# Performance work log

Measured on AMD Instinct MI355X. Metric: run time of the kernel, lower is better.

The kernel has to match this reference:

```python
import jax, jax.numpy as jnp
import numpy as np

EPS = 1e-15


def _trace(t):
    return jnp.einsum('bii->b', t)


def _ortho_loss(ss, k):
    n = jnp.linalg.norm(ss, axis=(-1, -2), keepdims=True)
    diff = ss / n - jnp.eye(k, dtype=ss.dtype) / np.float32(np.sqrt(k))
    return jnp.mean(jnp.linalg.norm(diff, axis=(-1, -2)))


def _mincut_terms(s, adj):
    out_adj = jnp.einsum('bnk,bnm,bml->bkl', s, adj, s)
    d_flat = adj.sum(-1)  # degrees [B,N]
    num = _trace(out_adj)
    den = _trace(jnp.einsum('bnk,bn,bnl->bkl', s, d_flat, s)) + EPS
    return out_adj, num, den, d_flat


def dense_mincut_rewiring(x, adj, s, mask):
    k = s.shape[-1]  # 2
    m = mask[..., None].astype(x.dtype)
    s = jax.nn.softmax(s, axis=-1) * m
    _, num, den, _ = _mincut_terms(s, adj)
    mincut_loss = -jnp.mean(num / den)
    ortho_loss = _ortho_loss(jnp.einsum('bnk,bnl->bkl', s, s), k)
    # laplacian derivative of spectral gap wrt A_uv: (f_u - f_v)^2, f = soft bipartition
    f = s[..., 0]
    dlam = (f[:, :, None] - f[:, None, :]) ** 2
    return adj * (1.0 - dlam), mincut_loss, ortho_loss


def dense_CT_rewiring(x, adj, s, mask):
    k = s.shape[-1]
    m = mask[..., None].astype(x.dtype)
    s = jax.nn.softmax(s, axis=-1) * m
    d_flat = adj.sum(-1)
    sds = _trace(jnp.einsum('bnk,bn,bnl->bkl', s, d_flat, s))
    sas = _trace(jnp.einsum('bnk,bnm,bml->bkl', s, adj, s))
    den = _trace(jnp.einsum('bnk,bnl->bkl', s, s)) + EPS
    ct_loss = jnp.mean((sds - sas) / den)  # tr(Z^T L Z) / tr(Z^T Z)
    ortho_loss = _ortho_loss(jnp.einsum('bnk,bnl->bkl', s, s), k)
    # pairwise CT distances ||z_u - z_v|| / vol(G), sparsified by A
    sq = (s * s).sum(-1)
    d2 = sq[:, :, None] + sq[:, None, :] - 2.0 * jnp.einsum('bnk,bmk->bnm', s, s)
    ct_dist = jnp.sqrt(jnp.maximum(d2, 0.0) + 1e-12)
    vol = d_flat.sum(-1)
    new_adj = (ct_dist / (vol[:, None, None] + EPS)) * adj
    return new_adj, ct_loss, ortho_loss


def dense_mincut_pool(x, adj, s, mask):
    k = s.shape[-1]
    m = mask[..., None].astype(x.dtype)
    s = jax.nn.softmax(s, axis=-1) * m
    x = x * m
    out = jnp.einsum('bnk,bnf->bkf', s, x)
    out_adj, num, den, _ = _mincut_terms(s, adj)
    mincut_loss = -jnp.mean(num / den)
    ortho_loss = _ortho_loss(jnp.einsum('bnk,bnl->bkl', s, s), k)
    out_adj = out_adj * (1.0 - jnp.eye(k, dtype=adj.dtype))  # zero diagonal
    d = jnp.sqrt(out_adj.sum(-1)) + EPS  # [B,k]
    out_adj = out_adj / d[:, None, :] / d[:, :, None]
    return out, out_adj, mincut_loss, ortho_loss


def _dgc(x, adj, w_rel, b_rel, w_root):
    # DenseGraphConv(aggr='add'): lin_rel(A @ x) + lin_root(x)
    return jnp.matmul(adj, x) @ w_rel + b_rel + x @ w_root


def setup_inputs() -> dict:
    B, N, IN, H, KC, OUT, KMC = 16, 1024, 128, 32, 32, 10, 16
    keys = iter(jax.random.split(jax.random.key(0), 48))

    def lin(fin, fout):
        lim = float(1.0 / np.sqrt(fin))
        return (jax.random.uniform(next(keys), (fin, fout), jnp.float32, -lim, lim),
                jax.random.uniform(next(keys), (fout,), jnp.float32, -lim, lim))

    x = jax.random.normal(next(keys), (B, N, IN), jnp.float32)
    u = jax.random.uniform(next(keys), (B, N, N), jnp.float32)
    a = (u < 0.0156).astype(jnp.float32)  # avg degree ~16
    adj = jnp.maximum(a, jnp.swapaxes(a, 1, 2)) * (1.0 - jnp.eye(N, dtype=jnp.float32))
    mask = jnp.ones((B, N), dtype=bool)
    W1, b1 = lin(IN, H)
    Wrw, brw = lin(H, 2)
    Wg_rel, bg = lin(H, H); Wg_root, _ = lin(H, H)
    Wmcg, bmcg = lin(H, KMC)
    W2g_rel, b2g = lin(H, H); W2g_root, _ = lin(H, H)
    Wct, bct = lin(H, KC)
    Wc_rel, bc = lin(H, H); Wc_root, _ = lin(H, H)
    Wmcc, bmcc = lin(H, KMC)
    Wcat, bcat = lin(2 * H, H)
    W2, b2 = lin(H, H)
    W3, b3 = lin(H, OUT)
    return dict(x=x, adj=adj, mask=mask, W1=W1, b1=b1, Wrw=Wrw, brw=brw,
                Wg_rel=Wg_rel, bg=bg, Wg_root=Wg_root, Wmcg=Wmcg, bmcg=bmcg,
                W2g_rel=W2g_rel, b2g=b2g, W2g_root=W2g_root, Wct=Wct, bct=bct,
                Wc_rel=Wc_rel, bc=bc, Wc_root=Wc_root, Wmcc=Wmcc, bmcc=bmcc,
                Wcat=Wcat, bcat=bcat, W2=W2, b2=b2, W3=W3, b3=b3)


def reference(x, adj, mask, W1, b1, Wrw, brw, Wg_rel, bg, Wg_root, Wmcg, bmcg,
              W2g_rel, b2g, W2g_root, Wct, bct, Wc_rel, bc, Wc_root, Wmcc, bmcc,
              Wcat, bcat, W2, b2, W3, b3):
    x = x @ W1 + b1
    # GAP branch
    adj_gap, mc_rw, ol_rw = dense_mincut_rewiring(x, adj, x @ Wrw + brw, mask)
    x_gap = _dgc(x, adj_gap, Wg_rel, bg, Wg_root)
    x_gap, adj_gap, mc1, ol1 = dense_mincut_pool(x_gap, adj_gap, x_gap @ Wmcg + bmcg, mask)
    x_gap = _dgc(x_gap, adj_gap, W2g_rel, b2g, W2g_root)
    # CT branch
    adj_ct, ct_loss, ol_ct = dense_CT_rewiring(x, adj, x @ Wct + bct, mask)
    x_ct = _dgc(x, adj_ct, Wc_rel, bc, Wc_root)
    x_ct, adj_ct, mc2, ol2 = dense_mincut_pool(x_ct, adj_ct, x_ct @ Wmcc + bmcc, mask)
    x_ct = _dgc(x_ct, adj_ct, W2g_rel, b2g, W2g_root)  # source reuses self.conv2gap here
    h = jax.nn.relu(jnp.concatenate([x_gap, x_ct], axis=2) @ Wcat + bcat).sum(axis=1)
    h = jax.nn.relu(h @ W2 + b2)
    logits = h @ W3 + b3
    main_loss = mc_rw + ct_loss + mc1 + mc2
    ortho_loss = ol_rw + ol_ct + ol1 + ol2
    return (jax.nn.log_softmax(logits, axis=-1), main_loss, ortho_loss)
```

## Files before the change

kernel.cpp:

```cpp
#include <hip/hip_runtime.h>
#include <math.h>

#define BB   16
#define NNODE 1024
#define INF_ 128
#define HH   32
#define KMC  16
#define CAP  128
#define EPS15 1e-15f

typedef float v4f __attribute__((ext_vector_type(4)));

#define OFF_X      0
#define OFF_SRW    524288
#define OFF_SQCT   557056
#define OFF_SCT    573440
#define OFF_D      1097728
#define OFF_NUMRW  1114112
#define OFF_SAS    1130496
#define OFF_DGAP   1146880
#define OFF_DCT    1163264
#define OFF_YGAP   1179648
#define OFF_YCT    1703936
#define OFF_XGAP   2228224
#define OFF_XCT    2752512
#define OFF_S2G    3276800
#define OFF_S2C    3538944
#define OFF_TG     3801088
#define OFF_TC     4063232
#define OFF_FROB   4325376
#define OFF_VOL    4325888
#define OFF_MCRW   4325904
#define OFF_CTB    4325920
#define OFF_OLRW   4325936
#define OFF_OLCT   4325952
#define OFF_MC1    4325968
#define OFF_MC2    4325984
#define OFF_OL1    4326000
#define OFF_OL2    4326016
#define OFF_OUTG   4326032
#define OFF_OUTC   4334224
#define OFF_G2G    4342416
#define OFF_G2C    4346512
#define OFF_OAG    4350608
#define OFF_OAC    4354704
#define OFF_ENNZ   4358800
#define OFF_EIDX   4375184
#define OFF_EWG    5423760
#define OFF_EWC    7520912
#define OFF_PACK   9618064

__device__ __forceinline__ float wave_sum(float v) {
#pragma unroll
  for (int off = 32; off >= 1; off >>= 1) v += __shfl_xor(v, off, 64);
  return v;
}

__device__ __forceinline__ float blk_sum(float v, float* sred, int tid) {
  v = wave_sum(v);
  __syncthreads();
  if ((tid & 63) == 0) sred[tid >> 6] = v;
  __syncthreads();
  return sred[0] + sred[1] + sred[2] + sred[3];
}

__device__ __forceinline__ void blk_sum17(float* v, float (*sm)[4], int tid) {
  int w = tid >> 6, lane = tid & 63;
#pragma unroll
  for (int i = 0; i < 17; i++) {
#pragma unroll
    for (int off = 32; off >= 1; off >>= 1) v[i] += __shfl_xor(v[i], off, 64);
  }
  if (lane == 0) {
#pragma unroll
    for (int i = 0; i < 17; i++) sm[i][w] = v[i];
  }
  __syncthreads();
#pragma unroll
  for (int i = 0; i < 17; i++) v[i] = sm[i][0] + sm[i][1] + sm[i][2] + sm[i][3];
}

__global__ __launch_bounds__(256) void k_fused0(
    const float* __restrict__ adj, const float* __restrict__ x,
    const float* __restrict__ W1, const float* __restrict__ b1,
    const float* __restrict__ Wrw, const float* __restrict__ brw,
    const float* __restrict__ Wct, const float* __restrict__ bct,
    float* __restrict__ ws)
{
  __shared__ __align__(16) float sW1[INF_*HH];
  __shared__ __align__(16) float sWct[HH*HH];
  __shared__ float sWrw[HH*2];
  __shared__ float sb1[HH], sbct[HH], sbrw[2];
  __shared__ __align__(16) float sx[8*INF_];
  __shared__ float sX[8*HH];
  __shared__ unsigned int s_e32[4][4][CAP/2];
  int tid = threadIdx.x;
  if (blockIdx.x < 1024) {
    int w = tid >> 6, lane = tid & 63;
    int row0 = blockIdx.x * 16 + w * 4;
    v4f v[16];
#pragma unroll
    for (int rr = 0; rr < 4; rr++) {
      const v4f* ar = (const v4f*)(adj + (size_t)(row0 + rr) * NNODE);
#pragma unroll
      for (int it = 0; it < 4; it++)
        v[rr*4 + it] = __builtin_nontemporal_load(&ar[it*64 + lane]);
    }
#pragma unroll
    for (int rr = 0; rr < 4; rr++) {
      int row = row0 + rr;
      int c = 0;
#pragma unroll
      for (int it = 0; it < 4; it++) {
        v4f a4 = v[rr*4 + it];
        c += (a4.x != 0.f) + (a4.y != 0.f) + (a4.z != 0.f) + (a4.w != 0.f);
      }
      int p = c;
#pragma unroll
      for (int off = 1; off < 64; off <<= 1) {
        int t = __shfl_up(p, off, 64);
        if (lane >= off) p += t;
      }
      int excl = p - c;
      int total = __shfl(p, 63, 64);
      unsigned short* es = (unsigned short*)s_e32[w][rr];
      int pos = excl;
#pragma unroll
      for (int it = 0; it < 4; it++) {
        v4f a4 = v[rr*4 + it];
        int m0 = it*256 + lane*4;
        if (a4.x != 0.f) { if (pos < CAP) es[pos] = (unsigned short)(m0+0); pos++; }
        if (a4.y != 0.f) { if (pos < CAP) es[pos] = (unsigned short)(m0+1); pos++; }
        if (a4.z != 0.f) { if (pos < CAP) es[pos] = (unsigned short)(m0+2); pos++; }
        if (a4.w != 0.f) { if (pos < CAP) es[pos] = (unsigned short)(m0+3); pos++; }
      }
      int nnzc = total < CAP ? total : CAP;
      __syncthreads();
      unsigned int* dst = (unsigned int*)((unsigned short*)(ws + OFF_EIDX) + (size_t)row*CAP);
      int n32 = (nnzc + 1) >> 1;
      if (lane < n32) dst[lane] = s_e32[w][rr][lane];
      if (lane == 0) {
        ((int*)(ws + OFF_ENNZ))[row] = nnzc;
        ws[OFF_D + row] = (float)total;
      }
    }
  } else {
    for (int i = tid; i < INF_*HH/4; i += 256)
      ((float4*)sW1)[i] = ((const float4*)W1)[i];
    ((float4*)sWct)[tid] = ((const float4*)Wct)[tid];
    if (tid < HH*2) sWrw[tid] = Wrw[tid];
    if (tid < HH) { sb1[tid] = b1[tid]; sbct[tid] = bct[tid]; }
    if (tid < 2) sbrw[tid] = brw[tid];
    size_t row0 = (size_t)(blockIdx.x - 1024) * 8;
    ((float4*)sx)[tid] = ((const float4*)(x + row0 * INF_))[tid];
    __syncthreads();
    int r = tid >> 5, h = tid & 31;
    float acc = sb1[h];
#pragma unroll 8
    for (int k = 0; k < INF_; k++) acc += sx[r*INF_ + k] * sW1[k*HH + h];
    size_t row = row0 + r;
    ws[OFF_X + row*HH + h] = acc;
    sX[r*HH + h] = acc;
    __syncthreads();
    float sraw = sbct[h];
#pragma unroll
    for (int k = 0; k < HH; k++) sraw += sX[r*HH + k] * sWct[k*HH + h];
    float mx = sraw;
#pragma unroll
    for (int off = 16; off >= 1; off >>= 1) mx = fmaxf(mx, __shfl_xor(mx, off, 32));
    float e = __expf(sraw - mx);
    float sum = e;
#pragma unroll
    for (int off = 16; off >= 1; off >>= 1) sum += __shfl_xor(sum, off, 32);
    float sv = e / sum;
    ws[OFF_SCT + row*HH + h] = sv;
    float sq = sv * sv;
#pragma unroll
    for (int off = 16; off >= 1; off >>= 1) sq += __shfl_xor(sq, off, 32);
    float xv = sX[r*HH + h];
    float t0 = xv * sWrw[h*2 + 0];
    float t1 = xv * sWrw[h*2 + 1];
#pragma unroll
    for (int off = 16; off >= 1; off >>= 1) { t0 += __shfl_xor(t0, off, 32); t1 += __shfl_xor(t1, off, 32); }
    if (h == 0) {
      ws[OFF_SQCT + row] = sq;
      float r0 = t0 + sbrw[0], r1 = t1 + sbrw[1];
      float m2 = fmaxf(r0, r1);
      float e0 = __expf(r0 - m2), e1 = __expf(r1 - m2);
      float inv = 1.0f / (e0 + e1);
      float s0 = e0*inv, s1 = e1*inv;
      ((float2*)(ws + OFF_SRW))[row] = make_float2(s0, s1);
      ((float4*)(ws + OFF_PACK))[row] = make_float4(s0, s1, sq, 0.f);
    }
  }
}

__global__ __launch_bounds__(256) void k_edgefeat(
    const float* __restrict__ Wg_rel, const float* __restrict__ bg, const float* __restrict__ Wg_root,
    const float* __restrict__ Wc_rel, const float* __restrict__ bc, const float* __restrict__ Wc_root,
    const float* __restrict__ Wmcg, const float* __restrict__ bmcg,
    const float* __restrict__ Wmcc, const float* __restrict__ bmcc,
    float* __restrict__ out, float* __restrict__ ws)
{
  __shared__ int   s_m[4][CAP];
  __shared__ float s_wg[4][CAP];
  __shared__ float s_wc[4][CAP];
  __shared__ float sp[8][32];
  __shared__ float sred[4];
  __shared__ __align__(16) float sWgrel[HH*HH], sWgroot[HH*HH], sWcrel[HH*HH], sWcroot[HH*HH];
  __shared__ __align__(16) float sWmcg[HH*KMC], sWmcc[HH*KMC];
  __shared__ float sbg[HH], sbc[HH], sbmcg[KMC], sbmcc[KMC];
  __shared__ float sYg[4*HH], sYc[4*HH], sXr[4*HH], sxg[4*HH], sxc[4*HH];
  int tid = threadIdx.x;
  if (blockIdx.x < 4096) {
    int xcd = blockIdx.x & 7;
    int idx = blockIdx.x >> 3;
    int b = xcd*2 + (idx >> 8);
    int chunk = idx & 255;
    int base4 = b*NNODE + chunk*4;
    ((float4*)sWgrel)[tid]  = ((const float4*)Wg_rel)[tid];
    ((float4*)sWgroot)[tid] = ((const float4*)Wg_root)[tid];
    ((float4*)sWcrel)[tid]  = ((const float4*)Wc_rel)[tid];
    ((float4*)sWcroot)[tid] = ((const float4*)Wc_root)[tid];
    if (tid < 128) { ((float4*)sWmcg)[tid] = ((const float4*)Wmcg)[tid];
                     ((float4*)sWmcc)[tid] = ((const float4*)Wmcc)[tid]; }
    if (tid < HH)  { sbg[tid] = bg[tid]; sbc[tid] = bc[tid]; }
    if (tid < KMC) { sbmcg[tid] = bmcg[tid]; sbmcc[tid] = bmcc[tid]; }
    if (tid < 128) sXr[tid] = ws[OFF_X + (size_t)base4*HH + tid];
    float vp = 0.f;
#pragma unroll
    for (int i = 0; i < 4; i++) vp += ws[OFF_D + (size_t)b*NNODE + tid + i*256];

    const float* X = ws + OFF_X;
    const float2* srw = (const float2*)(ws + OFF_SRW);
    const float* sqct = ws + OFF_SQCT;
    const float* sct = ws + OFF_SCT;
    const float4* pack = (const float4*)(ws + OFF_PACK) + (size_t)b*NNODE;
    int w = tid >> 6, lane = tid & 63;
    int row = base4 + w;
    int nnz = ((const int*)(ws + OFF_ENNZ))[row];
    const unsigned short* eidx = (const unsigned short*)(ws + OFF_EIDX) + (size_t)row*CAP;
    const float4* cn4 = (const float4*)(sct + (size_t)row * HH);
    float4 c[8];
#pragma unroll
    for (int i = 0; i < 8; i++) c[i] = cn4[i];
    float2 srwn = srw[row];
    float f_n = srwn.x;
    float sq_n = sqct[row];
    float numrw_p = 0.f, sas_p = 0.f, dg_p = 0.f, dc_p = 0.f;
    for (int e = lane; e < nnz; e += 64) {
      int m = eidx[e];
      s_m[w][e] = m;
      const float4* cm4 = (const float4*)(sct + ((size_t)b*NNODE + m) * HH);
      float dot = 0.f;
#pragma unroll
      for (int i = 0; i < 8; i++) {
        float4 d4 = cm4[i];
        dot += c[i].x*d4.x + c[i].y*d4.y + c[i].z*d4.z + c[i].w*d4.w;
      }
      float4 pk = pack[m];
      numrw_p += srwn.x*pk.x + srwn.y*pk.y;
      float df = f_n - pk.x;
      float wg = 1.0f - df*df;
      float d2 = sq_n + pk.z - 2.0f*dot;
      float wc = sqrtf(fmaxf(d2, 0.0f) + 1e-12f);
      sas_p += dot;
      dg_p += wg;
      dc_p += wc;
      s_wg[w][e] = wg;
      s_wc[w][e] = wc;
      size_t eo = (size_t)row*CAP + e;
      ws[OFF_EWG + eo] = wg;
      ws[OFF_EWC + eo] = wc;
    }
    float numrw = wave_sum(numrw_p);
    float sas = wave_sum(sas_p);
    float dgp = wave_sum(dg_p);
    float dcp = wave_sum(dc_p);
    if (lane == 0) {
      ws[OFF_NUMRW + row] = numrw;
      ws[OFF_SAS + row] = sas;
      ws[OFF_DGAP + row] = dgp;
      ws[OFF_DCT + row] = dcp;
    }
    __syncthreads();
    int eoff = lane >> 4, hp = lane & 15;
    float yg0 = 0.f, yg1 = 0.f, yc0 = 0.f, yc1 = 0.f;
    for (int e = eoff; e < nnz; e += 4) {
      int m = s_m[w][e];
      float wg = s_wg[w][e], wc = s_wc[w][e];
      float2 xv = ((const float2*)(X + ((size_t)b*NNODE + m)*HH))[hp];
      yg0 += wg*xv.x; yg1 += wg*xv.y;
      yc0 += wc*xv.x; yc1 += wc*xv.y;
    }
    yg0 += __shfl_xor(yg0, 16, 64); yg0 += __shfl_xor(yg0, 32, 64);
    yg1 += __shfl_xor(yg1, 16, 64); yg1 += __shfl_xor(yg1, 32, 64);
    yc0 += __shfl_xor(yc0, 16, 64); yc0 += __shfl_xor(yc0, 32, 64);
    yc1 += __shfl_xor(yc1, 16, 64); yc1 += __shfl_xor(yc1, 32, 64);
    if (eoff == 0) {
      sYg[w*HH + 2*hp] = yg0; sYg[w*HH + 2*hp + 1] = yg1;
      sYc[w*HH + 2*hp] = yc0; sYc[w*HH + 2*hp + 1] = yc1;
    }
    float vol = blk_sum(vp, sred, tid);
    float ivol = 1.0f / (vol + EPS15);
    if (tid < 128) {
      int r = tid >> 5, h = tid & 31;
      float accg = 0.f, accg2 = 0.f, accc = 0.f, accc2 = 0.f;
#pragma unroll
      for (int k = 0; k < HH; k++) {
        float ygv = sYg[r*HH + k], Xv = sXr[r*HH + k], ycv = sYc[r*HH + k];
        accg  += ygv * sWgrel[k*HH + h];
        accg2 += Xv  * sWgroot[k*HH + h];
        accc  += ycv * sWcrel[k*HH + h];
        accc2 += Xv  * sWcroot[k*HH + h];
      }
      float xgv = sbg[h] + accg + accg2;
      float xcv = sbc[h] + ivol*accc + accc2;
      size_t rw = (size_t)base4 + r;
      ws[OFF_XGAP + rw*HH + h] = xgv;
      ws[OFF_XCT  + rw*HH + h] = xcv;
      sxg[r*HH + h] = xgv;
      sxc[r*HH + h] = xcv;
    }
    __syncthreads();
    if (tid < 128) {
      int r = tid >> 5, h = tid & 31;
      int j = h & 15, halfsel = h >> 4;
      const float* sin_ = halfsel ? sxc : sxg;
      const float* sw = halfsel ? sWmcc : sWmcg;
      float raw = halfsel ? sbmcc[j] : sbmcg[j];
#pragma unroll
      for (int k = 0; k < HH; k++) raw += sin_[r*HH + k] * sw[k*KMC + j];
      float mx = raw;
#pragma unroll
      for (int off = 8; off >= 1; off >>= 1) mx = fmaxf(mx, __shfl_xor(mx, off, 16));
      float e = __expf(raw - mx);
      float sum = e;
#pragma unroll
      for (int off = 8; off >= 1; off >>= 1) sum += __shfl_xor(sum, off, 16);
      float sv = e / sum;
      size_t rw = (size_t)base4 + r;
      if (halfsel == 0) ws[OFF_S2G + rw*KMC + j] = sv;
      else              ws[OFF_S2C + rw*KMC + j] = sv;
    }
  } else if (blockIdx.x < 4608) {
    int blk = blockIdx.x - 4096;
    int xcd = blk & 7;
    int idx = blk >> 3;
    int b = xcd*2 + (idx >> 5);
    int i = idx & 31;
    const float* sct = ws + OFF_SCT + (size_t)b*NNODE*HH;
    int j = tid & 31, seg = tid >> 5;
    float acc = 0.f;
    for (int n = seg*128; n < seg*128 + 128; n++)
      acc += sct[n*HH + i] * sct[n*HH + j];
    sp[seg][j] = acc;
    __syncthreads();
    if (tid < 32) {
      float g = 0.f;
#pragma unroll
      for (int s = 0; s < 8; s++) g += sp[s][tid];
      float p = g * g;
#pragma unroll
      for (int off = 16; off >= 1; off >>= 1) p += __shfl_xor(p, off, 32);
      if (tid == 0) ws[OFF_FROB + b*32 + i] = p;
    }
  } else {
    int b = blockIdx.x - 4608;
    if (b == 0 && tid < 2) out[160 + tid] = 0.f;
    for (int i = tid; i < 2048; i += 256) ws[OFF_OUTG + b*2048 + i] = 0.f;
    float vp = 0.f;
    for (int n = tid; n < NNODE; n += 256) vp += ws[OFF_D + (size_t)b*NNODE + n];
    float vol = blk_sum(vp, sred, tid);
    if (tid == 0) ws[OFF_VOL + b] = vol;
  }
}

__global__ __launch_bounds__(512) void k_passred(float* __restrict__ ws)
{
  __shared__ float sg[32*16], sc[32*16], stg[32*16], stc[32*16];
  __shared__ float sxg[32*32], sxc[32*32];
  int b = blockIdx.x >> 5, chunk = blockIdx.x & 31;
  int tid = threadIdx.x;
  size_t n0 = (size_t)b * NNODE + chunk * 32;
  const float* pG  = ws + OFF_S2G  + n0 * KMC;
  const float* pC  = ws + OFF_S2C  + n0 * KMC;
  const float* pXG = ws + OFF_XGAP + n0 * HH;
  const float* pXC = ws + OFF_XCT  + n0 * HH;
  sg[tid] = pG[tid];
  sc[tid] = pC[tid];
  sxg[tid] = pXG[tid]; sxg[tid + 512] = pXG[tid + 512];
  sxc[tid] = pXC[tid]; sxc[tid + 512] = pXC[tid + 512];
  int w = tid >> 6, lane = tid & 63;
  int grp = lane >> 5;
  int sl  = (lane >> 4) & 1;
  int k   = lane & 15;
  const float* S2 = ws + (grp ? OFF_S2C : OFF_S2G) + (size_t)b * NNODE * KMC;
  float* sT = grp ? stc : stg;
#pragma unroll
  for (int i = 0; i < 4; i++) {
    int rr = w * 4 + i;
    size_t row = n0 + rr;
    int nnz = ((const int*)(ws + OFF_ENNZ))[row];
    const unsigned short* eidx = (const unsigned short*)(ws + OFF_EIDX) + row * CAP;
    const float* ew = ws + (grp ? OFF_EWC : OFF_EWG) + row * CAP;
    float acc = 0.f;
    int e = sl;
    for (; e + 2 < nnz; e += 4) {
      int m0 = eidx[e], m1 = eidx[e + 2];
      float w0 = ew[e], w1 = ew[e + 2];
      acc += w0 * S2[(size_t)m0 * KMC + k] + w1 * S2[(size_t)m1 * KMC + k];
    }
    if (e < nnz) acc += ew[e] * S2[(size_t)eidx[e] * KMC + k];
    acc += __shfl_xor(acc, 16, 32);
    if (sl == 0) sT[rr * 16 + k] = acc;
  }
  __syncthreads();
  int sub = tid >> 8, t = tid & 255;
  { int k0 = t >> 5, h0 = t & 31;
    float og0 = 0.f, og1 = 0.f, oc0 = 0.f, oc1 = 0.f;
#pragma unroll
    for (int i = 0; i < 16; i++) {
      int r = sub * 16 + i;
      float xgv = sxg[r*32 + h0], xcv = sxc[r*32 + h0];
      og0 += sg[r*16 + k0]     * xgv;
      og1 += sg[r*16 + k0 + 8] * xgv;
      oc0 += sc[r*16 + k0]     * xcv;
      oc1 += sc[r*16 + k0 + 8] * xcv;
    }
    atomicAdd(&ws[OFF_OUTG + b*512 + k0*32 + h0],     og0);
    atomicAdd(&ws[OFF_OUTG + b*512 + (k0+8)*32 + h0], og1);
    atomicAdd(&ws[OFF_OUTC + b*512 + k0*32 + h0],     oc0);
    atomicAdd(&ws[OFF_OUTC + b*512 + (k0+8)*32 + h0], oc1);
  }
  { int kk = t >> 4, l = t & 15;
    float gg = 0.f, gc = 0.f, ag = 0.f, ac = 0.f;
#pragma unroll
    for (int i = 0; i < 16; i++) {
      int r = sub * 16 + i;
      float sgk = sg[r*16 + kk], sck = sc[r*16 + kk];
      gg += sgk * sg [r*16 + l];
      gc += sck * sc [r*16 + l];
      ag += sgk * stg[r*16 + l];
      ac += sck * stc[r*16 + l];
    }
    atomicAdd(&ws[OFF_G2G + b*256 + t], gg);
    atomicAdd(&ws[OFF_G2C + b*256 + t], gc);
    atomicAdd(&ws[OFF_OAG + b*256 + t], ag);
    atomicAdd(&ws[OFF_OAC + b*256 + t], ac);
  }
}

__global__ __launch_bounds__(256) void k_batch2(
    const float* __restrict__ W2g_rel, const float* __restrict__ b2g, const float* __restrict__ W2g_root,
    const float* __restrict__ Wcat, const float* __restrict__ bcat,
    const float* __restrict__ W2, const float* __restrict__ b2,
    const float* __restrict__ W3, const float* __restrict__ b3,
    float* __restrict__ out, float* __restrict__ ws)
{
  __shared__ float sOAg[256], sOAc[256], sOutg[512], sOutc[512];
  __shared__ float sW2grel[1024], sW2groot[1024], sWcat[2048], sW2l[1024];
  __shared__ float sPg[512], sPc[512], sXg2[512], sXc2[512], sHt[512];
  __shared__ float sHs[32], sH2[32], sLg[16], sScal[2];
  __shared__ float sdkg[16], sdkc[16];
  __shared__ float smm[17][4];
  int b = blockIdx.x, tid = threadIdx.x;
  sOAg[tid] = ws[OFF_OAG + b*256 + tid];
  sOAc[tid] = ws[OFF_OAC + b*256 + tid];
  sOutg[tid]       = ws[OFF_OUTG + b*512 + tid];
  sOutg[tid + 256] = ws[OFF_OUTG + b*512 + tid + 256];
  sOutc[tid]       = ws[OFF_OUTC + b*512 + tid];
  sOutc[tid + 256] = ws[OFF_OUTC + b*512 + tid + 256];
  for (int i = tid; i < 1024; i += 256) { sW2grel[i] = W2g_rel[i]; sW2groot[i] = W2g_root[i]; sW2l[i] = W2[i]; }
  for (int i = tid; i < 2048; i += 256) sWcat[i] = Wcat[i];
  size_t base = (size_t)b * NNODE;
  const float2* srw = (const float2*)(ws + OFF_SRW);
  float v[17];
#pragma unroll
  for (int i = 0; i < 17; i++) v[i] = 0.f;
  for (int n = tid; n < NNODE; n += 256) {
    float dg = ws[OFF_DGAP + base + n], dc = ws[OFF_DCT + base + n];
    const float* pg = ws + OFF_S2G + (base + n)*KMC;
    const float* pc = ws + OFF_S2C + (base + n)*KMC;
    float ng = 0.f, nc = 0.f;
#pragma unroll
    for (int j = 0; j < KMC; j++) { ng += pg[j]*pg[j]; nc += pc[j]*pc[j]; }
    v[0] += dg * ng; v[1] += dc * nc; v[2] += ng; v[3] += nc;
    float d = ws[OFF_D + base + n];
    float2 s = srw[base + n];
    float sq = ws[OFF_SQCT + base + n];
    v[4] += d * (s.x*s.x + s.y*s.y);
    v[5] += ws[OFF_NUMRW + base + n];
    v[6] += d * sq;
    v[7] += ws[OFF_SAS + base + n];
    v[8] += sq;
    v[9] += s.x*s.x; v[10] += s.x*s.y; v[11] += s.y*s.y;
  }
  v[12] = (tid < 32) ? ws[OFF_FROB + b*32 + tid] : 0.f;
  float gv = ws[OFF_G2G + b*256 + tid];
  float cv = ws[OFF_G2C + b*256 + tid];
  v[13] = gv*gv; v[14] = cv*cv;
  __syncthreads();
  v[15] = (tid < 16) ? sOAg[tid*17] : 0.f;
  v[16] = (tid < 16) ? sOAc[tid*17] : 0.f;
  blk_sum17(v, smm, tid);
  float den1 = v[0], den2u = v[1], trg = v[2], trc = v[3], denrw = v[4], num = v[5],
        sds = v[6], sas = v[7], denct = v[8], g00 = v[9], g01 = v[10], g11 = v[11],
        frob2 = v[12], frobg2 = v[13], frobc2 = v[14], num1 = v[15], num2u = v[16];
  float vol = ws[OFF_VOL + b];
  float ivol = 1.0f / (vol + EPS15);
  if (tid == 0) {
    float mcrw = -num / (denrw + EPS15);
    float ctb  = (sds - sas) / (denct + EPS15);
    float nrw = sqrtf(g00*g00 + 2.f*g01*g01 + g11*g11);
    float olrw = sqrtf(fmaxf(2.f - 2.f*(g00 + g11)/(nrw*1.41421356237f), 0.f));
    float nct = sqrtf(frob2);
    float olct = sqrtf(fmaxf(2.f - 2.f*denct/(nct*5.65685424949f), 0.f));
    float mc1 = -num1 / (den1 + EPS15);
    float mc2 = -(num2u*ivol) / (den2u*ivol + EPS15);
    float ol1 = sqrtf(fmaxf(2.f - 2.f*trg/(sqrtf(frobg2)*4.f), 0.f));
    float ol2 = sqrtf(fmaxf(2.f - 2.f*trc/(sqrtf(frobc2)*4.f), 0.f));
    atomicAdd(out + 160, (mcrw + ctb + mc1 + mc2) * 0.0625f);
    atomicAdd(out + 161, (olrw + olct + ol1 + ol2) * 0.0625f);
  }
  sOAc[tid] *= ivol;
  __syncthreads();
  if (tid < 16) { sOAg[tid*17] = 0.f; sOAc[tid*17] = 0.f; }
  __syncthreads();
  if (tid < 16) {
    float rg = 0.f, rc = 0.f;
#pragma unroll
    for (int l = 0; l < 16; l++) { rg += sOAg[tid*16 + l]; rc += sOAc[tid*16 + l]; }
    sdkg[tid] = sqrtf(rg) + EPS15;
    sdkc[tid] = sqrtf(rc) + EPS15;
  }
  __syncthreads();
  { int k = tid >> 4, l = tid & 15;
    sOAg[tid] /= (sdkg[k]*sdkg[l]);
    sOAc[tid] /= (sdkc[k]*sdkc[l]); }
  __syncthreads();
  { int k = tid >> 5, h = tid & 31;
    float p0 = 0, p1 = 0, q0 = 0, q1 = 0;
#pragma unroll
    for (int l = 0; l < 16; l++) {
      p0 += sOAg[k*16 + l] * sOutg[l*32 + h];
      p1 += sOAg[(k+8)*16 + l] * sOutg[l*32 + h];
      q0 += sOAc[k*16 + l] * sOutc[l*32 + h];
      q1 += sOAc[(k+8)*16 + l] * sOutc[l*32 + h];
    }
    sPg[k*32 + h] = p0; sPg[(k+8)*32 + h] = p1;
    sPc[k*32 + h] = q0; sPc[(k+8)*32 + h] = q1;
  }
  __syncthreads();
  { int k = tid >> 5, h = tid & 31;
    float bb2 = b2g[h];
    float a0 = bb2, a1 = bb2, c0 = bb2, c1 = bb2;
#pragma unroll
    for (int q = 0; q < 32; q++) {
      float wr = sW2grel[q*32 + h], wo = sW2groot[q*32 + h];
      a0 += sPg[k*32 + q]*wr + sOutg[k*32 + q]*wo;
      a1 += sPg[(k+8)*32 + q]*wr + sOutg[(k+8)*32 + q]*wo;
      c0 += sPc[k*32 + q]*wr + sOutc[k*32 + q]*wo;
      c1 += sPc[(k+8)*32 + q]*wr + sOutc[(k+8)*32 + q]*wo;
    }
    sXg2[k*32 + h] = a0; sXg2[(k+8)*32 + h] = a1;
    sXc2[k*32 + h] = c0; sXc2[(k+8)*32 + h] = c1;
  }
  __syncthreads();
  { int k = tid >> 5, h = tid & 31;
    float bb = bcat[h];
    float t0 = bb, t1 = bb;
#pragma unroll
    for (int q = 0; q < 32; q++) {
      float w1v = sWcat[q*32 + h], w2v = sWcat[(q+32)*32 + h];
      t0 += sXg2[k*32 + q]*w1v + sXc2[k*32 + q]*w2v;
      t1 += sXg2[(k+8)*32 + q]*w1v + sXc2[(k+8)*32 + q]*w2v;
    }
    sHt[k*32 + h] = fmaxf(t0, 0.f);
    sHt[(k+8)*32 + h] = fmaxf(t1, 0.f);
  }
  __syncthreads();
  if (tid < 32) {
    float s = 0.f;
#pragma unroll
    for (int k = 0; k < 16; k++) s += sHt[k*32 + tid];
    sHs[tid] = s;
  }
  __syncthreads();
  if (tid < 32) {
    float a = b2[tid];
#pragma unroll
    for (int q = 0; q < 32; q++) a += sHs[q]*sW2l[q*32 + tid];
    sH2[tid] = fmaxf(a, 0.f);
  }
  __syncthreads();
  if (tid < 10) {
    float a = b3[tid];
#pragma unroll
    for (int q = 0; q < 32; q++) a += sH2[q]*W3[q*10 + tid];
    sLg[tid] = a;
  }
  __syncthreads();
  if (tid == 0) {
    float m = sLg[0];
    for (int o = 1; o < 10; o++) m = fmaxf(m, sLg[o]);
    float se = 0.f;
    for (int o = 0; o < 10; o++) se += __expf(sLg[o] - m);
    sScal[0] = m; sScal[1] = logf(se);
  }
  __syncthreads();
  if (tid < 10) out[b*10 + tid] = sLg[tid] - sScal[0] - sScal[1];
}

extern "C" void kernel_launch(void* const* d_in, const int* in_sizes, int n_in,
                              void* d_out, int out_size, void* d_ws, size_t ws_size,
                              hipStream_t stream)
{
  const float* x       = (const float*)d_in[0];
  const float* adj     = (const float*)d_in[1];
  const float* W1      = (const float*)d_in[3];
  const float* b1      = (const float*)d_in[4];
  const float* Wrw     = (const float*)d_in[5];
  const float* brw     = (const float*)d_in[6];
  const float* Wg_rel  = (const float*)d_in[7];
  const float* bg      = (const float*)d_in[8];
  const float* Wg_root = (const float*)d_in[9];
  const float* Wmcg    = (const float*)d_in[10];
  const float* bmcg    = (const float*)d_in[11];
  const float* W2g_rel = (const float*)d_in[12];
  const float* b2g     = (const float*)d_in[13];
  const float* W2g_root= (const float*)d_in[14];
  const float* Wct     = (const float*)d_in[15];
  const float* bct     = (const float*)d_in[16];
  const float* Wc_rel  = (const float*)d_in[17];
  const float* bc      = (const float*)d_in[18];
  const float* Wc_root = (const float*)d_in[19];
  const float* Wmcc    = (const float*)d_in[20];
  const float* bmcc    = (const float*)d_in[21];
  const float* Wcat    = (const float*)d_in[22];
  const float* bcat    = (const float*)d_in[23];
  const float* W2      = (const float*)d_in[24];
  const float* b2      = (const float*)d_in[25];
  const float* W3      = (const float*)d_in[26];
  const float* b3      = (const float*)d_in[27];
  float* out = (float*)d_out;
  float* ws  = (float*)d_ws;

  k_fused0<<<dim3(3072), dim3(256), 0, stream>>>(adj, x, W1, b1, Wrw, brw, Wct, bct, ws);
  k_edgefeat<<<dim3(4624), dim3(256), 0, stream>>>(Wg_rel, bg, Wg_root, Wc_rel, bc, Wc_root,
                                                   Wmcg, bmcg, Wmcc, bmcc, out, ws);
  k_passred<<<dim3(512), dim3(512), 0, stream>>>(ws);
  k_batch2<<<dim3(16), dim3(256), 0, stream>>>(W2g_rel, b2g, W2g_root, Wcat, bcat,
                                               W2, b2, W3, b3, out, ws);
}
```

Baseline: 253.2 us.

## Split edge dot products across lane quads and move per-batch reductions upstream

In the edge-feature kernel, each edge's 32-wide dot product is now split across four lanes and combined with shuffles. The per-node hidden projection uses all 256 threads as two half-K partners instead of 128 threads. The mincut projection weights are read directly from global memory instead of being staged in shared memory, and one barrier is removed. The 12 per-batch reduction terms that k_batch2 used to compute by sweeping every node are now produced in an earlier kernel as per-block partial sums added atomically to a new workspace slot, which shrinks the serial tail kernel at the cost of extra atomics and more global reads in the earlier kernel.

```diff
diff --git a/kernel.cpp b/kernel.cpp
--- a/kernel.cpp
+++ b/kernel.cpp
@@ -20,24 +20,12 @@
 #define OFF_SAS    1130496
 #define OFF_DGAP   1146880
 #define OFF_DCT    1163264
-#define OFF_YGAP   1179648
-#define OFF_YCT    1703936
 #define OFF_XGAP   2228224
 #define OFF_XCT    2752512
 #define OFF_S2G    3276800
 #define OFF_S2C    3538944
-#define OFF_TG     3801088
-#define OFF_TC     4063232
 #define OFF_FROB   4325376
 #define OFF_VOL    4325888
-#define OFF_MCRW   4325904
-#define OFF_CTB    4325920
-#define OFF_OLRW   4325936
-#define OFF_OLCT   4325952
-#define OFF_MC1    4325968
-#define OFF_MC2    4325984
-#define OFF_OL1    4326000
-#define OFF_OL2    4326016
 #define OFF_OUTG   4326032
 #define OFF_OUTC   4334224
 #define OFF_G2G    4342416
@@ -49,6 +37,7 @@
 #define OFF_EWG    5423760
 #define OFF_EWC    7520912
 #define OFF_PACK   9618064
+#define OFF_BSUM   9683600
 
 __device__ __forceinline__ float wave_sum(float v) {
 #pragma unroll
@@ -56,6 +45,16 @@
   return v;
 }
 
+__device__ __forceinline__ void wave_sum4(float& a, float& b, float& c, float& d) {
+#pragma unroll
+  for (int off = 32; off >= 1; off >>= 1) {
+    a += __shfl_xor(a, off, 64);
+    b += __shfl_xor(b, off, 64);
+    c += __shfl_xor(c, off, 64);
+    d += __shfl_xor(d, off, 64);
+  }
+}
+
 __device__ __forceinline__ float blk_sum(float v, float* sred, int tid) {
   v = wave_sum(v);
   __syncthreads();
@@ -64,20 +63,20 @@
   return sred[0] + sred[1] + sred[2] + sred[3];
 }
 
-__device__ __forceinline__ void blk_sum17(float* v, float (*sm)[4], int tid) {
+__device__ __forceinline__ void blk_sum5(float* v, float (*sm)[4], int tid) {
   int w = tid >> 6, lane = tid & 63;
 #pragma unroll
-  for (int i = 0; i < 17; i++) {
+  for (int i = 0; i < 5; i++) {
 #pragma unroll
     for (int off = 32; off >= 1; off >>= 1) v[i] += __shfl_xor(v[i], off, 64);
   }
   if (lane == 0) {
 #pragma unroll
-    for (int i = 0; i < 17; i++) sm[i][w] = v[i];
-  }
-  __syncthreads();
-#pragma unroll
-  for (int i = 0; i < 17; i++) v[i] = sm[i][0] + sm[i][1] + sm[i][2] + sm[i][3];
+    for (int i = 0; i < 5; i++) sm[i][w] = v[i];
+  }
+  __syncthreads();
+#pragma unroll
+  for (int i = 0; i < 5; i++) v[i] = sm[i][0] + sm[i][1] + sm[i][2] + sm[i][3];
 }
 
 __global__ __launch_bounds__(256) void k_fused0(
@@ -202,14 +201,13 @@
     const float* __restrict__ Wmcc, const float* __restrict__ bmcc,
     float* __restrict__ out, float* __restrict__ ws)
 {
-  __shared__ int   s_m[4][CAP];
+  __shared__ unsigned short s_m[4][CAP];
   __shared__ float s_wg[4][CAP];
   __shared__ float s_wc[4][CAP];
   __shared__ float sp[8][32];
   __shared__ float sred[4];
   __shared__ __align__(16) float sWgrel[HH*HH], sWgroot[HH*HH], sWcrel[HH*HH], sWcroot[HH*HH];
-  __shared__ __align__(16) float sWmcg[HH*KMC], sWmcc[HH*KMC];
-  __shared__ float sbg[HH], sbc[HH], sbmcg[KMC], sbmcc[KMC];
+  __shared__ float sbg[HH], sbc[HH];
   __shared__ float sYg[4*HH], sYc[4*HH], sXr[4*HH], sxg[4*HH], sxc[4*HH];
   int tid = threadIdx.x;
   if (blockIdx.x < 4096) {
@@ -222,10 +220,7 @@
     ((float4*)sWgroot)[tid] = ((const float4*)Wg_root)[tid];
     ((float4*)sWcrel)[tid]  = ((const float4*)Wc_rel)[tid];
     ((float4*)sWcroot)[tid] = ((const float4*)Wc_root)[tid];
-    if (tid < 128) { ((float4*)sWmcg)[tid] = ((const float4*)Wmcg)[tid];
-                     ((float4*)sWmcc)[tid] = ((const float4*)Wmcc)[tid]; }
     if (tid < HH)  { sbg[tid] = bg[tid]; sbc[tid] = bc[tid]; }
-    if (tid < KMC) { sbmcg[tid] = bmcg[tid]; sbmcc[tid] = bmcc[tid]; }
     if (tid < 128) sXr[tid] = ws[OFF_X + (size_t)base4*HH + tid];
     float vp = 0.f;
 #pragma unroll
@@ -237,27 +232,24 @@
     const float* sct = ws + OFF_SCT;
     const float4* pack = (const float4*)(ws + OFF_PACK) + (size_t)b*NNODE;
     int w = tid >> 6, lane = tid & 63;
+    int tm = lane & 3;
     int row = base4 + w;
     int nnz = ((const int*)(ws + OFF_ENNZ))[row];
     const unsigned short* eidx = (const unsigned short*)(ws + OFF_EIDX) + (size_t)row*CAP;
     const float4* cn4 = (const float4*)(sct + (size_t)row * HH);
-    float4 c[8];
-#pragma unroll
-    for (int i = 0; i < 8; i++) c[i] = cn4[i];
+    float4 c0 = cn4[tm*2], c1 = cn4[tm*2 + 1];
     float2 srwn = srw[row];
     float f_n = srwn.x;
     float sq_n = sqct[row];
     float numrw_p = 0.f, sas_p = 0.f, dg_p = 0.f, dc_p = 0.f;
-    for (int e = lane; e < nnz; e += 64) {
+    for (int e = (lane >> 2); e < nnz; e += 16) {
       int m = eidx[e];
-      s_m[w][e] = m;
       const float4* cm4 = (const float4*)(sct + ((size_t)b*NNODE + m) * HH);
-      float dot = 0.f;
-#pragma unroll
-      for (int i = 0; i < 8; i++) {
-        float4 d4 = cm4[i];
-        dot += c[i].x*d4.x + c[i].y*d4.y + c[i].z*d4.z + c[i].w*d4.w;
-      }
+      float4 d0 = cm4[tm*2], d1 = cm4[tm*2 + 1];
+      float dot = c0.x*d0.x + c0.y*d0.y + c0.z*d0.z + c0.w*d0.w
+                + c1.x*d1.x + c1.y*d1.y + c1.z*d1.z + c1.w*d1.w;
+      dot += __shfl_xor(dot, 1, 64);
+      dot += __shfl_xor(dot, 2, 64);
       float4 pk = pack[m];
       numrw_p += srwn.x*pk.x + srwn.y*pk.y;
       float df = f_n - pk.x;
@@ -267,23 +259,22 @@
       sas_p += dot;
       dg_p += wg;
       dc_p += wc;
-      s_wg[w][e] = wg;
-      s_wc[w][e] = wc;
-      size_t eo = (size_t)row*CAP + e;
-      ws[OFF_EWG + eo] = wg;
-      ws[OFF_EWC + eo] = wc;
-    }
-    float numrw = wave_sum(numrw_p);
-    float sas = wave_sum(sas_p);
-    float dgp = wave_sum(dg_p);
-    float dcp = wave_sum(dc_p);
+      if (tm == 0) {
+        s_m[w][e] = (unsigned short)m;
+        s_wg[w][e] = wg;
+        s_wc[w][e] = wc;
+        size_t eo = (size_t)row*CAP + e;
+        ws[OFF_EWG + eo] = wg;
+        ws[OFF_EWC + eo] = wc;
+      }
+    }
+    wave_sum4(numrw_p, sas_p, dg_p, dc_p);
     if (lane == 0) {
-      ws[OFF_NUMRW + row] = numrw;
-      ws[OFF_SAS + row] = sas;
-      ws[OFF_DGAP + row] = dgp;
-      ws[OFF_DCT + row] = dcp;
-    }
-    __syncthreads();
+      ws[OFF_NUMRW + row] = numrw_p * 0.25f;
+      ws[OFF_SAS + row] = sas_p * 0.25f;
+      ws[OFF_DGAP + row] = dg_p * 0.25f;
+      ws[OFF_DCT + row] = dc_p * 0.25f;
+    }
     int eoff = lane >> 4, hp = lane & 15;
     float yg0 = 0.f, yg1 = 0.f, yc0 = 0.f, yc1 = 0.f;
     for (int e = eoff; e < nnz; e += 4) {
@@ -303,32 +294,42 @@
     }
     float vol = blk_sum(vp, sred, tid);
     float ivol = 1.0f / (vol + EPS15);
-    if (tid < 128) {
-      int r = tid >> 5, h = tid & 31;
+    {
+      int r = tid >> 6;
+      int h = (tid >> 1) & 31;
+      int half = tid & 1;
+      int kb = half * 16;
       float accg = 0.f, accg2 = 0.f, accc = 0.f, accc2 = 0.f;
 #pragma unroll
-      for (int k = 0; k < HH; k++) {
+      for (int kk = 0; kk < 16; kk++) {
+        int k = kb + kk;
         float ygv = sYg[r*HH + k], Xv = sXr[r*HH + k], ycv = sYc[r*HH + k];
         accg  += ygv * sWgrel[k*HH + h];
         accg2 += Xv  * sWgroot[k*HH + h];
         accc  += ycv * sWcrel[k*HH + h];
         accc2 += Xv  * sWcroot[k*HH + h];
       }
-      float xgv = sbg[h] + accg + accg2;
-      float xcv = sbc[h] + ivol*accc + accc2;
-      size_t rw = (size_t)base4 + r;
-      ws[OFF_XGAP + rw*HH + h] = xgv;
-      ws[OFF_XCT  + rw*HH + h] = xcv;
-      sxg[r*HH + h] = xgv;
-      sxc[r*HH + h] = xcv;
+      accg  += __shfl_xor(accg, 1, 64);
+      accg2 += __shfl_xor(accg2, 1, 64);
+      accc  += __shfl_xor(accc, 1, 64);
+      accc2 += __shfl_xor(accc2, 1, 64);
+      if (half == 0) {
+        float xgv = sbg[h] + accg + accg2;
+        float xcv = sbc[h] + ivol*accc + accc2;
+        size_t rw = (size_t)base4 + r;
+        ws[OFF_XGAP + rw*HH + h] = xgv;
+        ws[OFF_XCT  + rw*HH + h] = xcv;
+        sxg[r*HH + h] = xgv;
+        sxc[r*HH + h] = xcv;
+      }
     }
     __syncthreads();
     if (tid < 128) {
       int r = tid >> 5, h = tid & 31;
       int j = h & 15, halfsel = h >> 4;
       const float* sin_ = halfsel ? sxc : sxg;
-      const float* sw = halfsel ? sWmcc : sWmcg;
-      float raw = halfsel ? sbmcc[j] : sbmcg[j];
+      const float* sw = halfsel ? Wmcc : Wmcg;
+      float raw = halfsel ? bmcc[j] : bmcg[j];
 #pragma unroll
       for (int k = 0; k < HH; k++) raw += sin_[r*HH + k] * sw[k*KMC + j];
       float mx = raw;
@@ -368,6 +369,7 @@
   } else {
     int b = blockIdx.x - 4608;
     if (b == 0 && tid < 2) out[160 + tid] = 0.f;
+    if (tid < 12) ws[OFF_BSUM + b*12 + tid] = 0.f;
     for (int i = tid; i < 2048; i += 256) ws[OFF_OUTG + b*2048 + i] = 0.f;
     float vp = 0.f;
     for (int n = tid; n < NNODE; n += 256) vp += ws[OFF_D + (size_t)b*NNODE + n];
@@ -449,6 +451,41 @@
     atomicAdd(&ws[OFF_OAG + b*256 + t], ag);
     atomicAdd(&ws[OFF_OAC + b*256 + t], ac);
   }
+  if (tid < 32) {
+    size_t gn = n0 + tid;
+    float ng = 0.f, nc = 0.f;
+#pragma unroll
+    for (int j = 0; j < KMC; j++) {
+      float a = sg[tid*16 + j], c2 = sc[tid*16 + j];
+      ng += a*a; nc += c2*c2;
+    }
+    float dgv = ws[OFF_DGAP + gn];
+    float dcv = ws[OFF_DCT + gn];
+    float d   = ws[OFF_D + gn];
+    float2 s  = ((const float2*)(ws + OFF_SRW))[gn];
+    float sq  = ws[OFF_SQCT + gn];
+    float nmr = ws[OFF_NUMRW + gn];
+    float sasv= ws[OFF_SAS + gn];
+    float u0 = dgv*ng, u1 = dcv*nc, u2 = ng, u3 = nc;
+    float u4 = d*(s.x*s.x + s.y*s.y), u5 = nmr, u6 = d*sq, u7 = sasv;
+    float u8 = sq, u9 = s.x*s.x, u10 = s.x*s.y, u11 = s.y*s.y;
+#pragma unroll
+    for (int off = 16; off >= 1; off >>= 1) {
+      u0 += __shfl_xor(u0, off, 32);  u1 += __shfl_xor(u1, off, 32);
+      u2 += __shfl_xor(u2, off, 32);  u3 += __shfl_xor(u3, off, 32);
+      u4 += __shfl_xor(u4, off, 32);  u5 += __shfl_xor(u5, off, 32);
+      u6 += __shfl_xor(u6, off, 32);  u7 += __shfl_xor(u7, off, 32);
+      u8 += __shfl_xor(u8, off, 32);  u9 += __shfl_xor(u9, off, 32);
+      u10 += __shfl_xor(u10, off, 32); u11 += __shfl_xor(u11, off, 32);
+    }
+    if (tid == 0) {
+      float* bs = ws + OFF_BSUM + b*12;
+      atomicAdd(bs + 0, u0);  atomicAdd(bs + 1, u1);  atomicAdd(bs + 2, u2);
+      atomicAdd(bs + 3, u3);  atomicAdd(bs + 4, u4);  atomicAdd(bs + 5, u5);
+      atomicAdd(bs + 6, u6);  atomicAdd(bs + 7, u7);  atomicAdd(bs + 8, u8);
+      atomicAdd(bs + 9, u9);  atomicAdd(bs + 10, u10); atomicAdd(bs + 11, u11);
+    }
+  }
 }
 
 __global__ __launch_bounds__(256) void k_batch2(
@@ -463,7 +500,7 @@
   __shared__ float sPg[512], sPc[512], sXg2[512], sXc2[512], sHt[512];
   __shared__ float sHs[32], sH2[32], sLg[16], sScal[2];
   __shared__ float sdkg[16], sdkc[16];
-  __shared__ float smm[17][4];
+  __shared__ float smm[5][4];
   int b = blockIdx.x, tid = threadIdx.x;
   sOAg[tid] = ws[OFF_OAG + b*256 + tid];
   sOAc[tid] = ws[OFF_OAC + b*256 + tid];
@@ -473,43 +510,23 @@
   sOutc[tid + 256] = ws[OFF_OUTC + b*512 + tid + 256];
   for (int i = tid; i < 1024; i += 256) { sW2grel[i] = W2g_rel[i]; sW2groot[i] = W2g_root[i]; sW2l[i] = W2[i]; }
   for (int i = tid; i < 2048; i += 256) sWcat[i] = Wcat[i];
-  size_t base = (size_t)b * NNODE;
-  const float2* srw = (const float2*)(ws + OFF_SRW);
-  float v[17];
-#pragma unroll
-  for (int i = 0; i < 17; i++) v[i] = 0.f;
-  for (int n = tid; n < NNODE; n += 256) {
-    float dg = ws[OFF_DGAP + base + n], dc = ws[OFF_DCT + base + n];
-    const float* pg = ws + OFF_S2G + (base + n)*KMC;
-    const float* pc = ws + OFF_S2C + (base + n)*KMC;
-    float ng = 0.f, nc = 0.f;
-#pragma unroll
-    for (int j = 0; j < KMC; j++) { ng += pg[j]*pg[j]; nc += pc[j]*pc[j]; }
-    v[0] += dg * ng; v[1] += dc * nc; v[2] += ng; v[3] += nc;
-    float d = ws[OFF_D + base + n];
-    float2 s = srw[base + n];
-    float sq = ws[OFF_SQCT + base + n];
-    v[4] += d * (s.x*s.x + s.y*s.y);
-    v[5] += ws[OFF_NUMRW + base + n];
-    v[6] += d * sq;
-    v[7] += ws[OFF_SAS + base + n];
-    v[8] += sq;
-    v[9] += s.x*s.x; v[10] += s.x*s.y; v[11] += s.y*s.y;
-  }
-  v[12] = (tid < 32) ? ws[OFF_FROB + b*32 + tid] : 0.f;
+  float v[5];
+  v[0] = (tid < 32) ? ws[OFF_FROB + b*32 + tid] : 0.f;
   float gv = ws[OFF_G2G + b*256 + tid];
   float cv = ws[OFF_G2C + b*256 + tid];
-  v[13] = gv*gv; v[14] = cv*cv;
-  __syncthreads();
-  v[15] = (tid < 16) ? sOAg[tid*17] : 0.f;
-  v[16] = (tid < 16) ? sOAc[tid*17] : 0.f;
-  blk_sum17(v, smm, tid);
-  float den1 = v[0], den2u = v[1], trg = v[2], trc = v[3], denrw = v[4], num = v[5],
-        sds = v[6], sas = v[7], denct = v[8], g00 = v[9], g01 = v[10], g11 = v[11],
-        frob2 = v[12], frobg2 = v[13], frobc2 = v[14], num1 = v[15], num2u = v[16];
+  v[1] = gv*gv; v[2] = cv*cv;
+  __syncthreads();
+  v[3] = (tid < 16) ? sOAg[tid*17] : 0.f;
+  v[4] = (tid < 16) ? sOAc[tid*17] : 0.f;
+  blk_sum5(v, smm, tid);
+  float frob2 = v[0], frobg2 = v[1], frobc2 = v[2], num1 = v[3], num2u = v[4];
   float vol = ws[OFF_VOL + b];
   float ivol = 1.0f / (vol + EPS15);
   if (tid == 0) {
+    const float* bs = ws + OFF_BSUM + b*12;
+    float den1 = bs[0], den2u = bs[1], trg = bs[2], trc = bs[3];
+    float denrw = bs[4], num = bs[5], sds = bs[6], sas = bs[7], denct = bs[8];
+    float g00 = bs[9], g01 = bs[10], g11 = bs[11];
     float mcrw = -num / (denrw + EPS15);
     float ctb  = (sds - sas) / (denct + EPS15);
     float nrw = sqrtf(g00*g00 + 2.f*g01*g01 + g11*g11);
```

New measurement: 252.9 us. About the same (-0.1%).
